# Performance work log

Measured on AMD Instinct MI355X. Metric: run time of the kernel, lower is better.

Reference implementation:

```python
import jax, jax.numpy as jnp
import numpy as np

D_MODEL = 1024
NHEAD = 16
HEAD_DIM = D_MODEL // NHEAD  # 64
THETA = 10000.0


def apply_rope(t):
    # t: [B, H, S, D]. Interleaved-pair RoPE (lucidrains rotary-embedding-torch
    # rotate_queries_or_keys), positions = arange(S), theta = 10000.
    B, H, S, D = t.shape
    inv_freq = 1.0 / (THETA ** (jnp.arange(0, D, 2, dtype=jnp.float32) / D))  # [D/2]
    ang = jnp.arange(S, dtype=jnp.float32)[:, None] * inv_freq               # [S, D/2]
    cos = jnp.cos(ang).astype(t.dtype)
    sin = jnp.sin(ang).astype(t.dtype)
    tp = t.reshape(B, H, S, D // 2, 2)
    x1, x2 = tp[..., 0], tp[..., 1]
    rot = jnp.stack([x1 * cos - x2 * sin, x1 * sin + x2 * cos], axis=-1)
    return rot.reshape(B, H, S, D)


def setup_inputs() -> dict:
    key = jax.random.key(0)
    k0, k1, k2, k3, k4 = jax.random.split(key, 5)
    B, Sx, Sc = 2, 2048, 2048
    sc = 0.02  # weight init scale
    return {
        "x": jax.random.normal(k0, (B, Sx, D_MODEL), jnp.float32),
        "context": jax.random.normal(k1, (B, Sc, D_MODEL), jnp.float32),
        "Wq": jax.random.normal(k2, (D_MODEL, D_MODEL), jnp.float32) * sc,
        "Wv": jax.random.normal(k3, (D_MODEL, D_MODEL), jnp.float32) * sc,
        "Wo": jax.random.normal(k4, (D_MODEL, D_MODEL), jnp.float32) * sc,
        "bo": jnp.zeros((D_MODEL,), jnp.float32),
        "x_pos": jnp.arange(B * Sx, dtype=jnp.int64).reshape(B, Sx) % Sx,
        "context_pos": jnp.arange(B * Sc, dtype=jnp.int64).reshape(B, Sc) % Sc,
    }


def reference(x, context, Wq, Wv, Wo, bo, x_pos, context_pos):
    # x_pos/context_pos are unused when both streams use the internal
    # RotaryEmbedding (is_imu1=is_imu2=True), matching the original forward.
    B, Sx, _ = x.shape
    Sc = context.shape[1]
    q = (x @ Wq.T).reshape(B, Sx, NHEAD, HEAD_DIM).transpose(0, 2, 1, 3)
    # NOTE: original code uses projq (not projk) for keys — replicated here.
    k = (context @ Wq.T).reshape(B, Sc, NHEAD, HEAD_DIM).transpose(0, 2, 1, 3)
    v = (context @ Wv.T).reshape(B, Sc, NHEAD, HEAD_DIM).transpose(0, 2, 1, 3)
    q = apply_rope(q)
    k = apply_rope(k)
    scale = 1.0 / jnp.sqrt(jnp.asarray(HEAD_DIM, q.dtype))
    attn = jax.nn.softmax(jnp.einsum("bhqd,bhkd->bhqk", q, k) * scale, axis=-1)
    out = jnp.einsum("bhqk,bhkd->bhqd", attn, v)            # [B,H,Sx,hd]
    out = out.transpose(0, 2, 1, 3).reshape(B, Sx, D_MODEL)  # [B,Sx,d_model]
    return out @ Wo.T + bo
```

## Files before the change

### kernel.cpp

```cpp
#include <hip/hip_runtime.h>
#include <cmath>


typedef __bf16 bf16x8 __attribute__((ext_vector_type(8)));
typedef __bf16 bf16x4 __attribute__((ext_vector_type(4)));
typedef float f32x4 __attribute__((ext_vector_type(4)));

#define MFMA(A, B, C) __builtin_amdgcn_mfma_f32_16x16x32_bf16(A, B, C, 0, 0, 0)
#define GLL16(g, l)                                                        \
  __builtin_amdgcn_global_load_lds(                                        \
      (const __attribute__((address_space(1))) unsigned int*)(g),          \
      (__attribute__((address_space(3))) unsigned int*)(l), 16, 0, 0)

__global__ __launch_bounds__(256) void cvt_kernel(const float* __restrict__ src,
                                                  __bf16* __restrict__ dst, int n4) {
  int i = blockIdx.x * 256 + threadIdx.x;
  if (i < n4) {
    float4 f = ((const float4*)src)[i];
    bf16x4 o;
    o[0] = (__bf16)f.x; o[1] = (__bf16)f.y; o[2] = (__bf16)f.z; o[3] = (__bf16)f.w;
    ((bf16x4*)dst)[i] = o;
  }
}

template <int MODE>
__global__ __launch_bounds__(256) void gemm_bt(const __bf16* __restrict__ A,
                                               const __bf16* __restrict__ W,
                                               void* __restrict__ outp0,
                                               void* __restrict__ outp1,
                                               const float* __restrict__ bias) {
  const int tid = threadIdx.x;
  const int wave = tid >> 6, lane = tid & 63, quad = lane >> 4, l15 = lane & 15;
  const int mw = wave >> 1, nw = wave & 1;
  const int m0 = blockIdx.x * 128, n0 = blockIdx.y * 128;

  __shared__ __attribute__((aligned(16))) __bf16 As[2][4096];
  __shared__ __attribute__((aligned(16))) __bf16 Ws[2][4096];

  int goff[2];
#pragma unroll
  for (int jj = 0; jj < 2; jj++) {
    const int s = jj * 256 + tid;
    const int row = s >> 2;
    const int kcg = (s & 3) ^ ((row >> 1) & 3);
    goff[jj] = row * 1024 + kcg * 8;
  }
  const __bf16* Ag = A + (size_t)m0 * 1024;
  const __bf16* Wg = W + (size_t)n0 * 1024;
  const int ldsoff0 = (0 * 256 + wave * 64) * 8;
  const int ldsoff1 = (1 * 256 + wave * 64) * 8;

  const int sw = (l15 >> 1) & 3;
  int afoff[4], wfoff[4];
#pragma unroll
  for (int t = 0; t < 4; t++) {
    afoff[t] = (mw * 64 + t * 16 + l15) * 32 + (quad ^ sw) * 8;
    wfoff[t] = (nw * 64 + t * 16 + l15) * 32 + (quad ^ sw) * 8;
  }

  f32x4 acc[4][4] = {};

  auto stage = [&](int buf, int k0) {
    GLL16(Ag + goff[0] + k0, &As[buf][ldsoff0]);
    GLL16(Ag + goff[1] + k0, &As[buf][ldsoff1]);
    GLL16(Wg + goff[0] + k0, &Ws[buf][ldsoff0]);
    GLL16(Wg + goff[1] + k0, &Ws[buf][ldsoff1]);
  };
  auto compute = [&](int buf) {
    bf16x8 af[4], wf[4];
#pragma unroll
    for (int t = 0; t < 4; t++) af[t] = *(const bf16x8*)&As[buf][afoff[t]];
#pragma unroll
    for (int t = 0; t < 4; t++) wf[t] = *(const bf16x8*)&Ws[buf][wfoff[t]];
#pragma unroll
    for (int mt = 0; mt < 4; mt++)
#pragma unroll
      for (int nt = 0; nt < 4; nt++) acc[mt][nt] = MFMA(af[mt], wf[nt], acc[mt][nt]);
  };

  stage(0, 0);
  for (int k0 = 0; k0 < 1024; k0 += 64) {
    __syncthreads();
    if (k0 + 32 < 1024) stage(1, k0 + 32);
    compute(0);
    __syncthreads();
    if (k0 + 64 < 1024) stage(0, k0 + 64);
    compute(1);
  }

  if (MODE == 0) {
    const int stream = (m0 >= 4096);
    __bf16* O = (__bf16*)(stream ? outp1 : outp0);
    const float qsc = stream ? 1.0f : 0.18033688f;
    const int mb = m0 & 4095;
#pragma unroll
    for (int nt = 0; nt < 4; nt++) {
      const int n = n0 + nw * 64 + nt * 16 + l15;
      const int h = n >> 6, d = n & 63, p = d >> 1;
      const float invf = __builtin_amdgcn_exp2f(-(float)p * 0.41524101f);
#pragma unroll
      for (int mt = 0; mt < 4; mt++) {
#pragma unroll
        for (int r = 0; r < 4; r++) {
          const int row = mb + mw * 64 + mt * 16 + quad * 4 + r;
          const int s = row & 2047, b = row >> 11;
          float v = acc[mt][nt][r];
          float pv = __shfl_xor(v, 1, 64);
          float sn, cs;
          __sincosf((float)s * invf, &sn, &cs);
          float res = (lane & 1) ? (pv * sn + v * cs) : (v * cs - pv * sn);
          O[((size_t)(b * 16 + h) * 2048 + s) * 64 + d] = (__bf16)(res * qsc);
        }
      }
    }
  } else if (MODE == 1) {
    __bf16* O = (__bf16*)outp0;
#pragma unroll
    for (int nt = 0; nt < 4; nt++) {
      const int n = n0 + nw * 64 + nt * 16 + l15;
      const int h = n >> 6, d = n & 63;
#pragma unroll
      for (int mt = 0; mt < 4; mt++) {
        const int rowb = m0 + mw * 64 + mt * 16 + quad * 4;
        const int s = rowb & 2047, b = rowb >> 11;
        bf16x4 o;
#pragma unroll
        for (int r = 0; r < 4; r++) o[r] = (__bf16)acc[mt][nt][r];
        *(bf16x4*)(O + ((size_t)(b * 16 + h) * 64 + d) * 2048 + s) = o;
      }
    }
  } else {
    float* O = (float*)outp0;
#pragma unroll
    for (int nt = 0; nt < 4; nt++) {
      const int n = n0 + nw * 64 + nt * 16 + l15;
      const float bv = bias[n];
#pragma unroll
      for (int mt = 0; mt < 4; mt++) {
#pragma unroll
        for (int r = 0; r < 4; r++) {
          const int row = m0 + mw * 64 + mt * 16 + quad * 4 + r;
          O[(size_t)row * 1024 + n] = acc[mt][nt][r] + bv;
        }
      }
    }
  }
}

__global__ __launch_bounds__(256) void attn_kernel(const __bf16* __restrict__ Q,
                                                   const __bf16* __restrict__ K,
                                                   const __bf16* __restrict__ Vt,
                                                   __bf16* __restrict__ Aout) {
  const int tid = threadIdx.x;
  const int wave = tid >> 6, lane = tid & 63, quad = lane >> 4, l15 = lane & 15;
  const int q0 = blockIdx.x * 128;
  const int bh = blockIdx.y;

  const __bf16* Qb = Q + (size_t)bh * (2048 * 64);
  const __bf16* Kb = K + (size_t)bh * (2048 * 64);
  const __bf16* Vb = Vt + (size_t)bh * (64 * 2048);

  __shared__ __attribute__((aligned(16))) __bf16 Kbuf[2][4096];
  __shared__ __attribute__((aligned(16))) __bf16 Vbuf[2][4096];
  __shared__ __attribute__((aligned(16))) __bf16 Plds[4][2][8][16][8];

  bf16x8 qf[2][2];
#pragma unroll
  for (int c = 0; c < 2; c++) {
    const __bf16* qp = Qb + (size_t)(q0 + wave * 32 + c * 16 + l15) * 64 + quad * 8;
    qf[c][0] = *(const bf16x8*)qp;
    qf[c][1] = *(const bf16x8*)(qp + 32);
  }

  const int s0 = (wave * 2 + 0) * 64 + lane;
  const int s1 = (wave * 2 + 1) * 64 + lane;
  const int r0 = s0 >> 3, c0 = (s0 & 7) ^ (r0 & 7);
  const int r1 = s1 >> 3, c1 = (s1 & 7) ^ (r1 & 7);
  const __bf16* kg0 = Kb + r0 * 64 + c0 * 8;
  const __bf16* kg1 = Kb + r1 * 64 + c1 * 8;
  const __bf16* vg0 = Vb + r0 * 2048 + c0 * 8;
  const __bf16* vg1 = Vb + r1 * 2048 + c1 * 8;
  const int kldsA = (wave * 2 + 0) * 512;
  const int kldsB = (wave * 2 + 1) * 512;

  const int offF0 = l15 * 64 + ((quad ^ (l15 & 7)) * 8);
  const int offF1 = l15 * 64 + (((4 + quad) ^ (l15 & 7)) * 8);

  float rsum[2] = {0.f, 0.f};
  f32x4 oT[4][2] = {};

  auto stage = [&](int buf, int kt) {
    GLL16(kg0 + kt * 64, &Kbuf[buf][kldsA]);
    GLL16(kg1 + kt * 64, &Kbuf[buf][kldsB]);
    GLL16(vg0 + kt, &Vbuf[buf][kldsA]);
    GLL16(vg1 + kt, &Vbuf[buf][kldsB]);
  };
  auto compute = [&](int buf) {
    f32x4 sT[2][4];
#pragma unroll
    for (int nt = 0; nt < 4; nt++) {
      bf16x8 kf0 = *(const bf16x8*)&Kbuf[buf][nt * 1024 + offF0];
      bf16x8 kf1 = *(const bf16x8*)&Kbuf[buf][nt * 1024 + offF1];
#pragma unroll
      for (int c = 0; c < 2; c++) {
        f32x4 z = {};
        z = MFMA(kf0, qf[c][0], z);
        sT[c][nt] = MFMA(kf1, qf[c][1], z);
      }
    }
#pragma unroll
    for (int c = 0; c < 2; c++) {
#pragma unroll
      for (int nt = 0; nt < 4; nt++) {
        bf16x4 pb;
#pragma unroll
        for (int r = 0; r < 4; r++) {
          float pe = __builtin_amdgcn_exp2f(sT[c][nt][r]);
          rsum[c] += pe;
          pb[r] = (__bf16)pe;
        }
        const int chunk = nt * 2 + (quad >> 1);
        *(bf16x4*)&Plds[wave][c][chunk][l15 ^ ((chunk & 3) << 1)][(quad & 1) * 4] = pb;
      }
    }
    bf16x8 pf[2][2];
#pragma unroll
    for (int c = 0; c < 2; c++) {
      pf[c][0] = *(const bf16x8*)&Plds[wave][c][quad][l15 ^ (quad << 1)][0];
      pf[c][1] = *(const bf16x8*)&Plds[wave][c][4 + quad][l15 ^ (quad << 1)][0];
    }
#pragma unroll
    for (int nt = 0; nt < 4; nt++) {
      bf16x8 vf0 = *(const bf16x8*)&Vbuf[buf][nt * 1024 + offF0];
      bf16x8 vf1 = *(const bf16x8*)&Vbuf[buf][nt * 1024 + offF1];
#pragma unroll
      for (int c = 0; c < 2; c++) {
        oT[nt][c] = MFMA(vf0, pf[c][0], oT[nt][c]);
        oT[nt][c] = MFMA(vf1, pf[c][1], oT[nt][c]);
      }
    }
  };

  stage(0, 0);
  for (int kt = 0; kt < 2048; kt += 128) {
    __syncthreads();
    if (kt + 64 < 2048) stage(1, kt + 64);
    compute(0);
    __syncthreads();
    if (kt + 128 < 2048) stage(0, kt + 128);
    compute(1);
  }

  const int b = bh >> 4, h = bh & 15;
#pragma unroll
  for (int c = 0; c < 2; c++) {
    float l = rsum[c];
    l += __shfl_xor(l, 16, 64);
    l += __shfl_xor(l, 32, 64);
    const float inv = 1.f / l;
    const int q = q0 + wave * 32 + c * 16 + l15;
#pragma unroll
    for (int nt = 0; nt < 4; nt++) {
      bf16x4 o;
#pragma unroll
      for (int r = 0; r < 4; r++) o[r] = (__bf16)(oT[nt][c][r] * inv);
      *(bf16x4*)&Aout[((size_t)(b * 2048 + q)) * 1024 + h * 64 + nt * 16 + quad * 4] = o;
    }
  }
}

extern "C" void kernel_launch(void* const* d_in, const int* in_sizes, int n_in,
                              void* d_out, int out_size, void* d_ws, size_t ws_size,
                              hipStream_t stream) {
  const float* x   = (const float*)d_in[0];
  const float* ctx = (const float*)d_in[1];
  const float* Wq  = (const float*)d_in[2];
  const float* Wv  = (const float*)d_in[3];
  const float* Wo  = (const float*)d_in[4];
  const float* bo  = (const float*)d_in[5];

  char* ws = (char*)d_ws;
  const size_t MB = 1024 * 1024;
  __bf16* xb   = (__bf16*)(ws + 0 * MB);
  __bf16* cb   = (__bf16*)(ws + 8 * MB);
  __bf16* Wqb  = (__bf16*)(ws + 16 * MB);
  __bf16* Wvb  = (__bf16*)(ws + 18 * MB);
  __bf16* Wob  = (__bf16*)(ws + 20 * MB);
  __bf16* qh   = (__bf16*)(ws + 22 * MB);
  __bf16* kh   = (__bf16*)(ws + 30 * MB);
  __bf16* vt   = (__bf16*)(ws + 38 * MB);
  __bf16* attn = xb;

  cvt_kernel<<<4096, 256, 0, stream>>>(x,   xb,  1048576);
  cvt_kernel<<<4096, 256, 0, stream>>>(ctx, cb,  1048576);
  cvt_kernel<<<1024, 256, 0, stream>>>(Wq,  Wqb, 262144);
  cvt_kernel<<<1024, 256, 0, stream>>>(Wv,  Wvb, 262144);
  cvt_kernel<<<1024, 256, 0, stream>>>(Wo,  Wob, 262144);

  gemm_bt<0><<<dim3(64, 8), 256, 0, stream>>>(xb, Wqb, (void*)qh, (void*)kh, nullptr);
  gemm_bt<1><<<dim3(32, 8), 256, 0, stream>>>(cb, Wvb, (void*)vt, nullptr, nullptr);

  attn_kernel<<<dim3(16, 32), 256, 0, stream>>>(qh, kh, vt, attn);

  gemm_bt<2><<<dim3(32, 8), 256, 0, stream>>>(attn, Wob, d_out, nullptr, bo);
}
```

Before: 229.0 us.

## Merge conversion and QKV GEMM launches, halve attention query tile per block

The five fp32-to-bf16 conversion launches become one kernel that picks its source by global index. The V projection is folded into the Q/K GEMM launch through extra grid blocks, which relies on the workspace buffers for x/context and Wq/Wv sitting next to each other. The attention kernel now handles 16 query rows per wave instead of 32, which doubles the block count for better occupancy and load balance. The cost is that each block reuses every K/V tile staged in LDS across half as many queries.

```diff
diff --git a/kernel.cpp b/kernel.cpp
--- a/kernel.cpp
+++ b/kernel.cpp
@@ -12,27 +12,49 @@
       (const __attribute__((address_space(1))) unsigned int*)(g),          \
       (__attribute__((address_space(3))) unsigned int*)(l), 16, 0, 0)
 
-__global__ __launch_bounds__(256) void cvt_kernel(const float* __restrict__ src,
-                                                  __bf16* __restrict__ dst, int n4) {
+__global__ __launch_bounds__(256) void cvt_all_kernel(
+    const float* __restrict__ x, const float* __restrict__ ctx,
+    const float* __restrict__ Wq, const float* __restrict__ Wv,
+    const float* __restrict__ Wo, __bf16* __restrict__ xb, __bf16* __restrict__ cb,
+    __bf16* __restrict__ Wqb, __bf16* __restrict__ Wvb, __bf16* __restrict__ Wob) {
   int i = blockIdx.x * 256 + threadIdx.x;
-  if (i < n4) {
-    float4 f = ((const float4*)src)[i];
-    bf16x4 o;
-    o[0] = (__bf16)f.x; o[1] = (__bf16)f.y; o[2] = (__bf16)f.z; o[3] = (__bf16)f.w;
-    ((bf16x4*)dst)[i] = o;
-  }
+  const float* src;
+  __bf16* dst;
+  int off;
+  if (i < 1048576) { src = x; dst = xb; off = 0; }
+  else if (i < 2097152) { src = ctx; dst = cb; off = 1048576; }
+  else if (i < 2359296) { src = Wq; dst = Wqb; off = 2097152; }
+  else if (i < 2621440) { src = Wv; dst = Wvb; off = 2359296; }
+  else { src = Wo; dst = Wob; off = 2621440; }
+  int j = i - off;
+  float4 f = ((const float4*)src)[j];
+  bf16x4 o;
+  o[0] = (__bf16)f.x; o[1] = (__bf16)f.y; o[2] = (__bf16)f.z; o[3] = (__bf16)f.w;
+  ((bf16x4*)dst)[j] = o;
 }
 
 template <int MODE>
-__global__ __launch_bounds__(256) void gemm_bt(const __bf16* __restrict__ A,
-                                               const __bf16* __restrict__ W,
+__global__ __launch_bounds__(256) void gemm_bt(const __bf16* __restrict__ A0,
+                                               const __bf16* __restrict__ W0,
                                                void* __restrict__ outp0,
                                                void* __restrict__ outp1,
+                                               void* __restrict__ outp2,
                                                const float* __restrict__ bias) {
   const int tid = threadIdx.x;
   const int wave = tid >> 6, lane = tid & 63, quad = lane >> 4, l15 = lane & 15;
   const int mw = wave >> 1, nw = wave & 1;
-  const int m0 = blockIdx.x * 128, n0 = blockIdx.y * 128;
+  const int n0 = blockIdx.y * 128;
+
+  int m0 = blockIdx.x * 128;
+  const __bf16* A = A0;
+  const __bf16* W = W0;
+  bool vmode = false;
+  if (MODE == 0 && blockIdx.x >= 64) {
+    m0 = (blockIdx.x - 64) * 128;
+    A = A0 + (size_t)4096 * 1024;
+    W = W0 + (size_t)1024 * 1024;
+    vmode = true;
+  }
 
   __shared__ __attribute__((aligned(16))) __bf16 As[2][4096];
   __shared__ __attribute__((aligned(16))) __bf16 Ws[2][4096];
@@ -89,44 +111,46 @@
   }
 
   if (MODE == 0) {
-    const int stream = (m0 >= 4096);
-    __bf16* O = (__bf16*)(stream ? outp1 : outp0);
-    const float qsc = stream ? 1.0f : 0.18033688f;
-    const int mb = m0 & 4095;
-#pragma unroll
-    for (int nt = 0; nt < 4; nt++) {
-      const int n = n0 + nw * 64 + nt * 16 + l15;
-      const int h = n >> 6, d = n & 63, p = d >> 1;
-      const float invf = __builtin_amdgcn_exp2f(-(float)p * 0.41524101f);
-#pragma unroll
-      for (int mt = 0; mt < 4; mt++) {
-#pragma unroll
-        for (int r = 0; r < 4; r++) {
-          const int row = mb + mw * 64 + mt * 16 + quad * 4 + r;
-          const int s = row & 2047, b = row >> 11;
-          float v = acc[mt][nt][r];
-          float pv = __shfl_xor(v, 1, 64);
-          float sn, cs;
-          __sincosf((float)s * invf, &sn, &cs);
-          float res = (lane & 1) ? (pv * sn + v * cs) : (v * cs - pv * sn);
-          O[((size_t)(b * 16 + h) * 2048 + s) * 64 + d] = (__bf16)(res * qsc);
+    if (!vmode) {
+      const int stream = (m0 >= 4096);
+      __bf16* O = (__bf16*)(stream ? outp1 : outp0);
+      const float qsc = stream ? 1.0f : 0.18033688f;
+      const int mb = m0 & 4095;
+#pragma unroll
+      for (int nt = 0; nt < 4; nt++) {
+        const int n = n0 + nw * 64 + nt * 16 + l15;
+        const int h = n >> 6, d = n & 63, p = d >> 1;
+        const float invf = __builtin_amdgcn_exp2f(-(float)p * 0.41524101f);
+#pragma unroll
+        for (int mt = 0; mt < 4; mt++) {
+#pragma unroll
+          for (int r = 0; r < 4; r++) {
+            const int row = mb + mw * 64 + mt * 16 + quad * 4 + r;
+            const int s = row & 2047, b = row >> 11;
+            float v = acc[mt][nt][r];
+            float pv = __shfl_xor(v, 1, 64);
+            float sn, cs;
+            __sincosf((float)s * invf, &sn, &cs);
+            float res = (lane & 1) ? (pv * sn + v * cs) : (v * cs - pv * sn);
+            O[((size_t)(b * 16 + h) * 2048 + s) * 64 + d] = (__bf16)(res * qsc);
+          }
         }
       }
-    }
-  } else if (MODE == 1) {
-    __bf16* O = (__bf16*)outp0;
-#pragma unroll
-    for (int nt = 0; nt < 4; nt++) {
-      const int n = n0 + nw * 64 + nt * 16 + l15;
-      const int h = n >> 6, d = n & 63;
-#pragma unroll
-      for (int mt = 0; mt < 4; mt++) {
-        const int rowb = m0 + mw * 64 + mt * 16 + quad * 4;
-        const int s = rowb & 2047, b = rowb >> 11;
-        bf16x4 o;
-#pragma unroll
-        for (int r = 0; r < 4; r++) o[r] = (__bf16)acc[mt][nt][r];
-        *(bf16x4*)(O + ((size_t)(b * 16 + h) * 64 + d) * 2048 + s) = o;
+    } else {
+      __bf16* O = (__bf16*)outp2;
+#pragma unroll
+      for (int nt = 0; nt < 4; nt++) {
+        const int n = n0 + nw * 64 + nt * 16 + l15;
+        const int h = n >> 6, d = n & 63;
+#pragma unroll
+        for (int mt = 0; mt < 4; mt++) {
+          const int rowb = m0 + mw * 64 + mt * 16 + quad * 4;
+          const int s = rowb & 2047, b = rowb >> 11;
+          bf16x4 o;
+#pragma unroll
+          for (int r = 0; r < 4; r++) o[r] = (__bf16)acc[mt][nt][r];
+          *(bf16x4*)(O + ((size_t)(b * 16 + h) * 64 + d) * 2048 + s) = o;
+        }
       }
     }
   } else {
@@ -153,7 +177,7 @@
                                                    __bf16* __restrict__ Aout) {
   const int tid = threadIdx.x;
   const int wave = tid >> 6, lane = tid & 63, quad = lane >> 4, l15 = lane & 15;
-  const int q0 = blockIdx.x * 128;
+  const int q0 = blockIdx.x * 64;
   const int bh = blockIdx.y;
 
   const __bf16* Qb = Q + (size_t)bh * (2048 * 64);
@@ -162,15 +186,11 @@
 
   __shared__ __attribute__((aligned(16))) __bf16 Kbuf[2][4096];
   __shared__ __attribute__((aligned(16))) __bf16 Vbuf[2][4096];
-  __shared__ __attribute__((aligned(16))) __bf16 Plds[4][2][8][16][8];
-
-  bf16x8 qf[2][2];
-#pragma unroll
-  for (int c = 0; c < 2; c++) {
-    const __bf16* qp = Qb + (size_t)(q0 + wave * 32 + c * 16 + l15) * 64 + quad * 8;
-    qf[c][0] = *(const bf16x8*)qp;
-    qf[c][1] = *(const bf16x8*)(qp + 32);
-  }
+  __shared__ __attribute__((aligned(16))) __bf16 Plds[4][8][16][8];
+
+  const __bf16* qp = Qb + (size_t)(q0 + wave * 16 + l15) * 64 + quad * 8;
+  const bf16x8 qf0 = *(const bf16x8*)qp;
+  const bf16x8 qf1 = *(const bf16x8*)(qp + 32);
 
   const int s0 = (wave * 2 + 0) * 64 + lane;
   const int s1 = (wave * 2 + 1) * 64 + lane;
@@ -186,8 +206,8 @@
   const int offF0 = l15 * 64 + ((quad ^ (l15 & 7)) * 8);
   const int offF1 = l15 * 64 + (((4 + quad) ^ (l15 & 7)) * 8);
 
-  float rsum[2] = {0.f, 0.f};
-  f32x4 oT[4][2] = {};
+  float rsum = 0.f;
+  f32x4 oT[4] = {};
 
   auto stage = [&](int buf, int kt) {
     GLL16(kg0 + kt * 64, &Kbuf[buf][kldsA]);
@@ -196,48 +216,35 @@
     GLL16(vg1 + kt, &Vbuf[buf][kldsB]);
   };
   auto compute = [&](int buf) {
-    f32x4 sT[2][4];
+    f32x4 sT[4];
 #pragma unroll
     for (int nt = 0; nt < 4; nt++) {
       bf16x8 kf0 = *(const bf16x8*)&Kbuf[buf][nt * 1024 + offF0];
       bf16x8 kf1 = *(const bf16x8*)&Kbuf[buf][nt * 1024 + offF1];
-#pragma unroll
-      for (int c = 0; c < 2; c++) {
-        f32x4 z = {};
-        z = MFMA(kf0, qf[c][0], z);
-        sT[c][nt] = MFMA(kf1, qf[c][1], z);
+      f32x4 z = {};
+      z = MFMA(kf0, qf0, z);
+      sT[nt] = MFMA(kf1, qf1, z);
+    }
+#pragma unroll
+    for (int nt = 0; nt < 4; nt++) {
+      bf16x4 pb;
+#pragma unroll
+      for (int r = 0; r < 4; r++) {
+        float pe = __builtin_amdgcn_exp2f(sT[nt][r]);
+        rsum += pe;
+        pb[r] = (__bf16)pe;
       }
-    }
-#pragma unroll
-    for (int c = 0; c < 2; c++) {
-#pragma unroll
-      for (int nt = 0; nt < 4; nt++) {
-        bf16x4 pb;
-#pragma unroll
-        for (int r = 0; r < 4; r++) {
-          float pe = __builtin_amdgcn_exp2f(sT[c][nt][r]);
-          rsum[c] += pe;
-          pb[r] = (__bf16)pe;
-        }
-        const int chunk = nt * 2 + (quad >> 1);
-        *(bf16x4*)&Plds[wave][c][chunk][l15 ^ ((chunk & 3) << 1)][(quad & 1) * 4] = pb;
-      }
-    }
-    bf16x8 pf[2][2];
-#pragma unroll
-    for (int c = 0; c < 2; c++) {
-      pf[c][0] = *(const bf16x8*)&Plds[wave][c][quad][l15 ^ (quad << 1)][0];
-      pf[c][1] = *(const bf16x8*)&Plds[wave][c][4 + quad][l15 ^ (quad << 1)][0];
-    }
+      const int chunk = nt * 2 + (quad >> 1);
+      *(bf16x4*)&Plds[wave][chunk][l15 ^ ((chunk & 3) << 1)][(quad & 1) * 4] = pb;
+    }
+    bf16x8 pf0 = *(const bf16x8*)&Plds[wave][quad][l15 ^ (quad << 1)][0];
+    bf16x8 pf1 = *(const bf16x8*)&Plds[wave][4 + quad][l15 ^ (quad << 1)][0];
 #pragma unroll
     for (int nt = 0; nt < 4; nt++) {
       bf16x8 vf0 = *(const bf16x8*)&Vbuf[buf][nt * 1024 + offF0];
       bf16x8 vf1 = *(const bf16x8*)&Vbuf[buf][nt * 1024 + offF1];
-#pragma unroll
-      for (int c = 0; c < 2; c++) {
-        oT[nt][c] = MFMA(vf0, pf[c][0], oT[nt][c]);
-        oT[nt][c] = MFMA(vf1, pf[c][1], oT[nt][c]);
-      }
+      oT[nt] = MFMA(vf0, pf0, oT[nt]);
+      oT[nt] = MFMA(vf1, pf1, oT[nt]);
     }
   };
 
@@ -252,20 +259,17 @@
   }
 
   const int b = bh >> 4, h = bh & 15;
-#pragma unroll
-  for (int c = 0; c < 2; c++) {
-    float l = rsum[c];
-    l += __shfl_xor(l, 16, 64);
-    l += __shfl_xor(l, 32, 64);
-    const float inv = 1.f / l;
-    const int q = q0 + wave * 32 + c * 16 + l15;
-#pragma unroll
-    for (int nt = 0; nt < 4; nt++) {
-      bf16x4 o;
-#pragma unroll
-      for (int r = 0; r < 4; r++) o[r] = (__bf16)(oT[nt][c][r] * inv);
-      *(bf16x4*)&Aout[((size_t)(b * 2048 + q)) * 1024 + h * 64 + nt * 16 + quad * 4] = o;
-    }
+  float l = rsum;
+  l += __shfl_xor(l, 16, 64);
+  l += __shfl_xor(l, 32, 64);
+  const float inv = 1.f / l;
+  const int q = q0 + wave * 16 + l15;
+#pragma unroll
+  for (int nt = 0; nt < 4; nt++) {
+    bf16x4 o;
+#pragma unroll
+    for (int r = 0; r < 4; r++) o[r] = (__bf16)(oT[nt][r] * inv);
+    *(bf16x4*)&Aout[((size_t)(b * 2048 + q)) * 1024 + h * 64 + nt * 16 + quad * 4] = o;
   }
 }
 
@@ -291,16 +295,12 @@
   __bf16* vt   = (__bf16*)(ws + 38 * MB);
   __bf16* attn = xb;
 
-  cvt_kernel<<<4096, 256, 0, stream>>>(x,   xb,  1048576);
-  cvt_kernel<<<4096, 256, 0, stream>>>(ctx, cb,  1048576);
-  cvt_kernel<<<1024, 256, 0, stream>>>(Wq,  Wqb, 262144);
-  cvt_kernel<<<1024, 256, 0, stream>>>(Wv,  Wvb, 262144);
-  cvt_kernel<<<1024, 256, 0, stream>>>(Wo,  Wob, 262144);
-
-  gemm_bt<0><<<dim3(64, 8), 256, 0, stream>>>(xb, Wqb, (void*)qh, (void*)kh, nullptr);
-  gemm_bt<1><<<dim3(32, 8), 256, 0, stream>>>(cb, Wvb, (void*)vt, nullptr, nullptr);
-
-  attn_kernel<<<dim3(16, 32), 256, 0, stream>>>(qh, kh, vt, attn);
-
-  gemm_bt<2><<<dim3(32, 8), 256, 0, stream>>>(attn, Wob, d_out, nullptr, bo);
+  cvt_all_kernel<<<11264, 256, 0, stream>>>(x, ctx, Wq, Wv, Wo, xb, cb, Wqb, Wvb, Wob);
+
+  gemm_bt<0><<<dim3(96, 8), 256, 0, stream>>>(xb, Wqb, (void*)qh, (void*)kh,
+                                              (void*)vt, nullptr);
+
+  attn_kernel<<<dim3(32, 32), 256, 0, stream>>>(qh, kh, vt, attn);
+
+  gemm_bt<2><<<dim3(32, 8), 256, 0, stream>>>(attn, Wob, d_out, nullptr, nullptr, bo);
 }
```

After: 221.6 us. 1.03x faster.

## Merge conversion and projection launches, remap attention grid, narrow output GEMM tile

Applied to the files above, without the earlier changes.

Five fp32-to-bf16 conversion launches become a single kernel that picks its source by flat index. The Q/K projection and the V projection are fused into one 96x8 grid launch that relies on xb/cb and Wqb/Wvb being contiguous in the workspace. The attention grid is flattened and remapped so consecutive blocks cover different heads. The output projection uses 128x64 tiles, doubling its block count to 512 for better CU fill on 256 CUs. The aim is fewer launches and better occupancy, at the cost of implicit layout assumptions and extra branching in the fused kernels.

```diff
diff --git a/kernel.cpp b/kernel.cpp
--- a/kernel.cpp
+++ b/kernel.cpp
@@ -12,27 +12,47 @@
       (const __attribute__((address_space(1))) unsigned int*)(g),          \
       (__attribute__((address_space(3))) unsigned int*)(l), 16, 0, 0)
 
-__global__ __launch_bounds__(256) void cvt_kernel(const float* __restrict__ src,
-                                                  __bf16* __restrict__ dst, int n4) {
+__global__ __launch_bounds__(256) void cvt_all_kernel(
+    const float* __restrict__ x, const float* __restrict__ ctx,
+    const float* __restrict__ Wq, const float* __restrict__ Wv,
+    const float* __restrict__ Wo, __bf16* __restrict__ xb, __bf16* __restrict__ cb,
+    __bf16* __restrict__ Wqb, __bf16* __restrict__ Wvb, __bf16* __restrict__ Wob) {
   int i = blockIdx.x * 256 + threadIdx.x;
-  if (i < n4) {
-    float4 f = ((const float4*)src)[i];
-    bf16x4 o;
-    o[0] = (__bf16)f.x; o[1] = (__bf16)f.y; o[2] = (__bf16)f.z; o[3] = (__bf16)f.w;
-    ((bf16x4*)dst)[i] = o;
-  }
-}
-
-template <int MODE>
-__global__ __launch_bounds__(256) void gemm_bt(const __bf16* __restrict__ A,
-                                               const __bf16* __restrict__ W,
-                                               void* __restrict__ outp0,
-                                               void* __restrict__ outp1,
-                                               const float* __restrict__ bias) {
+  const float* src;
+  __bf16* dst;
+  int off;
+  if (i < 1048576) { src = x; dst = xb; off = 0; }
+  else if (i < 2097152) { src = ctx; dst = cb; off = 1048576; }
+  else if (i < 2359296) { src = Wq; dst = Wqb; off = 2097152; }
+  else if (i < 2621440) { src = Wv; dst = Wvb; off = 2359296; }
+  else { src = Wo; dst = Wob; off = 2621440; }
+  int j = i - off;
+  float4 f = ((const float4*)src)[j];
+  bf16x4 o;
+  o[0] = (__bf16)f.x; o[1] = (__bf16)f.y; o[2] = (__bf16)f.z; o[3] = (__bf16)f.w;
+  ((bf16x4*)dst)[j] = o;
+}
+
+__global__ __launch_bounds__(256) void gemm_proj(const __bf16* __restrict__ A0,
+                                                 const __bf16* __restrict__ W0,
+                                                 void* __restrict__ outQ,
+                                                 void* __restrict__ outK,
+                                                 void* __restrict__ outV) {
   const int tid = threadIdx.x;
   const int wave = tid >> 6, lane = tid & 63, quad = lane >> 4, l15 = lane & 15;
   const int mw = wave >> 1, nw = wave & 1;
-  const int m0 = blockIdx.x * 128, n0 = blockIdx.y * 128;
+  const int n0 = blockIdx.y * 128;
+
+  int m0 = blockIdx.x * 128;
+  const __bf16* A = A0;
+  const __bf16* W = W0;
+  bool vmode = false;
+  if (blockIdx.x >= 64) {
+    m0 = (blockIdx.x - 64) * 128;
+    A = A0 + (size_t)4096 * 1024;
+    W = W0 + (size_t)1024 * 1024;
+    vmode = true;
+  }
 
   __shared__ __attribute__((aligned(16))) __bf16 As[2][4096];
   __shared__ __attribute__((aligned(16))) __bf16 Ws[2][4096];
@@ -47,8 +67,8 @@
   }
   const __bf16* Ag = A + (size_t)m0 * 1024;
   const __bf16* Wg = W + (size_t)n0 * 1024;
-  const int ldsoff0 = (0 * 256 + wave * 64) * 8;
-  const int ldsoff1 = (1 * 256 + wave * 64) * 8;
+  const int ldsoff0 = wave * 512;
+  const int ldsoff1 = 2048 + wave * 512;
 
   const int sw = (l15 >> 1) & 3;
   int afoff[4], wfoff[4];
@@ -88,10 +108,10 @@
     compute(1);
   }
 
-  if (MODE == 0) {
-    const int stream = (m0 >= 4096);
-    __bf16* O = (__bf16*)(stream ? outp1 : outp0);
-    const float qsc = stream ? 1.0f : 0.18033688f;
+  if (!vmode) {
+    const int isK = (m0 >= 4096);
+    __bf16* O = (__bf16*)(isK ? outK : outQ);
+    const float qsc = isK ? 1.0f : 0.18033688f;
     const int mb = m0 & 4095;
 #pragma unroll
     for (int nt = 0; nt < 4; nt++) {
@@ -113,8 +133,8 @@
         }
       }
     }
-  } else if (MODE == 1) {
-    __bf16* O = (__bf16*)outp0;
+  } else {
+    __bf16* O = (__bf16*)outV;
 #pragma unroll
     for (int nt = 0; nt < 4; nt++) {
       const int n = n0 + nw * 64 + nt * 16 + l15;
@@ -129,19 +149,82 @@
         *(bf16x4*)(O + ((size_t)(b * 16 + h) * 64 + d) * 2048 + s) = o;
       }
     }
-  } else {
-    float* O = (float*)outp0;
-#pragma unroll
-    for (int nt = 0; nt < 4; nt++) {
-      const int n = n0 + nw * 64 + nt * 16 + l15;
-      const float bv = bias[n];
-#pragma unroll
-      for (int mt = 0; mt < 4; mt++) {
-#pragma unroll
-        for (int r = 0; r < 4; r++) {
-          const int row = m0 + mw * 64 + mt * 16 + quad * 4 + r;
-          O[(size_t)row * 1024 + n] = acc[mt][nt][r] + bv;
-        }
+  }
+}
+
+__global__ __launch_bounds__(256) void gemm_out(const __bf16* __restrict__ A,
+                                                const __bf16* __restrict__ W,
+                                                float* __restrict__ O,
+                                                const float* __restrict__ bias) {
+  const int tid = threadIdx.x;
+  const int wave = tid >> 6, lane = tid & 63, quad = lane >> 4, l15 = lane & 15;
+  const int mw = wave >> 1, nw = wave & 1;
+  const int m0 = blockIdx.x * 128, n0 = blockIdx.y * 64;
+
+  __shared__ __attribute__((aligned(16))) __bf16 As[2][4096];
+  __shared__ __attribute__((aligned(16))) __bf16 Ws[2][2048];
+
+  int goff[2];
+#pragma unroll
+  for (int jj = 0; jj < 2; jj++) {
+    const int s = jj * 256 + tid;
+    const int row = s >> 2;
+    const int kcg = (s & 3) ^ ((row >> 1) & 3);
+    goff[jj] = row * 1024 + kcg * 8;
+  }
+  const __bf16* Ag = A + (size_t)m0 * 1024;
+  const __bf16* Wg = W + (size_t)n0 * 1024;
+  const int ldsoff0 = wave * 512;
+  const int ldsoff1 = 2048 + wave * 512;
+
+  const int sw = (l15 >> 1) & 3;
+  int afoff[4], wfoff[2];
+#pragma unroll
+  for (int t = 0; t < 4; t++)
+    afoff[t] = (mw * 64 + t * 16 + l15) * 32 + (quad ^ sw) * 8;
+#pragma unroll
+  for (int t = 0; t < 2; t++)
+    wfoff[t] = (nw * 32 + t * 16 + l15) * 32 + (quad ^ sw) * 8;
+
+  f32x4 acc[4][2] = {};
+
+  auto stage = [&](int buf, int k0) {
+    GLL16(Ag + goff[0] + k0, &As[buf][ldsoff0]);
+    GLL16(Ag + goff[1] + k0, &As[buf][ldsoff1]);
+    GLL16(Wg + goff[0] + k0, &Ws[buf][ldsoff0]);
+  };
+  auto compute = [&](int buf) {
+    bf16x8 af[4], wf[2];
+#pragma unroll
+    for (int t = 0; t < 4; t++) af[t] = *(const bf16x8*)&As[buf][afoff[t]];
+#pragma unroll
+    for (int t = 0; t < 2; t++) wf[t] = *(const bf16x8*)&Ws[buf][wfoff[t]];
+#pragma unroll
+    for (int mt = 0; mt < 4; mt++)
+#pragma unroll
+      for (int nt = 0; nt < 2; nt++) acc[mt][nt] = MFMA(af[mt], wf[nt], acc[mt][nt]);
+  };
+
+  stage(0, 0);
+  for (int k0 = 0; k0 < 1024; k0 += 64) {
+    __syncthreads();
+    if (k0 + 32 < 1024) stage(1, k0 + 32);
+    compute(0);
+    __syncthreads();
+    if (k0 + 64 < 1024) stage(0, k0 + 64);
+    compute(1);
+  }
+
+#pragma unroll
+  for (int nt = 0; nt < 2; nt++) {
+    const int n = n0 + nw * 32 + nt * 16 + l15;
+    const float bv = bias[n];
+#pragma unroll
+    for (int mt = 0; mt < 4; mt++) {
+#pragma unroll
+      for (int r = 0; r < 4; r++) {
+        const int row = m0 + mw * 64 + mt * 16 + quad * 4 + r;
+        O[(size_t)row * 1024 + n] = acc[mt][nt][r] + bv;
       }
     }
   }
@@ -153,8 +236,10 @@
                                                    __bf16* __restrict__ Aout) {
   const int tid = threadIdx.x;
   const int wave = tid >> 6, lane = tid & 63, quad = lane >> 4, l15 = lane & 15;
-  const int q0 = blockIdx.x * 128;
-  const int bh = blockIdx.y;
+  const int id = blockIdx.x;
+  const int j = id >> 3;
+  const int bh = ((id & 7) << 2) | (j & 3);
+  const int q0 = (j >> 2) << 7;
 
   const __bf16* Qb = Q + (size_t)bh * (2048 * 64);
   const __bf16* Kb = K + (size_t)bh * (2048 * 64);
@@ -291,16 +376,11 @@
   __bf16* vt   = (__bf16*)(ws + 38 * MB);
   __bf16* attn = xb;
 
-  cvt_kernel<<<4096, 256, 0, stream>>>(x,   xb,  1048576);
-  cvt_kernel<<<4096, 256, 0, stream>>>(ctx, cb,  1048576);
-  cvt_kernel<<<1024, 256, 0, stream>>>(Wq,  Wqb, 262144);
-  cvt_kernel<<<1024, 256, 0, stream>>>(Wv,  Wvb, 262144);
-  cvt_kernel<<<1024, 256, 0, stream>>>(Wo,  Wob, 262144);
-
-  gemm_bt<0><<<dim3(64, 8), 256, 0, stream>>>(xb, Wqb, (void*)qh, (void*)kh, nullptr);
-  gemm_bt<1><<<dim3(32, 8), 256, 0, stream>>>(cb, Wvb, (void*)vt, nullptr, nullptr);
-
-  attn_kernel<<<dim3(16, 32), 256, 0, stream>>>(qh, kh, vt, attn);
-
-  gemm_bt<2><<<dim3(32, 8), 256, 0, stream>>>(attn, Wob, d_out, nullptr, bo);
-}
+  cvt_all_kernel<<<11264, 256, 0, stream>>>(x, ctx, Wq, Wv, Wo, xb, cb, Wqb, Wvb, Wob);
+
+  gemm_proj<<<dim3(96, 8), 256, 0, stream>>>(xb, Wqb, (void*)qh, (void*)kh, (void*)vt);
+
+  attn_kernel<<<512, 256, 0, stream>>>(qh, kh, vt, attn);
+
+  gemm_out<<<dim3(32, 16), 256, 0, stream>>>(attn, Wob, (float*)d_out, bo);
+}
```

Measured after the change: 216.2 us. 5.6% less time.
